# Optimization experiments

Hardware: AMD Instinct MI355X
Metric: run time of the kernel (lower is better)

Reference implementation:

```python
import jax, jax.numpy as jnp
import numpy as np
from jax import lax

VALUE_RANGE = (0.0, 1.0)
NUM_PARAMS = 1
ENC_DIM = 256


def conv2d(x, W, b, stride, pad):
    y = lax.conv_general_dilated(x, W, (stride, stride), [(pad, pad), (pad, pad)],
                                 dimension_numbers=("NCHW", "OIHW", "NCHW"))
    return y + b[None, :, None, None]


def min_pool2d(x, r):
    # torch: -max_pool2d(-x, k=2r+1, stride=1, pad=r)  == min pool padded with +inf
    k = 2 * r + 1
    return lax.reduce_window(x, jnp.inf, lax.min, (1, 1, k, k), (1, 1, 1, 1),
                             padding=[(0, 0), (0, 0), (r, r), (r, r)])


def setup_inputs() -> dict:
    key = jax.random.key(0)
    ks = jax.random.split(key, 10)
    x = jax.random.uniform(ks[0], (16, 3, 512, 512), dtype=jnp.float32)
    latent_out = jax.random.normal(ks[1], (16, ENC_DIM, 32, 32), dtype=jnp.float32)
    W1 = jax.random.normal(ks[2], (ENC_DIM // 2, ENC_DIM, 3, 3), dtype=jnp.float32) * 0.02
    b1 = jnp.zeros((ENC_DIM // 2,), jnp.float32)
    W2 = jax.random.normal(ks[3], (NUM_PARAMS, ENC_DIM // 2, 3, 3), dtype=jnp.float32) * 0.05
    b2 = jnp.zeros((NUM_PARAMS,), jnp.float32)
    W3 = jax.random.normal(ks[4], (NUM_PARAMS, NUM_PARAMS, 1, 1), dtype=jnp.float32) * 0.5
    b3 = jnp.zeros((NUM_PARAMS,), jnp.float32)
    return {"x": x, "latent_out": latent_out, "W1": W1, "b1": b1,
            "W2": W2, "b2": b2, "W3": W3, "b3": b3}


def reference(x, latent_out, W1, b1, W2, b2, W3, b3):
    n, c, H, W = x.shape
    # ---- params_predictor ----
    h = conv2d(latent_out, W1, b1, 2, 1)
    h = jnp.where(h >= 0, h, 0.02 * h)  # LeakyReLU(0.02)
    h = conv2d(h, W2, b2, 2, 1)
    h = h.mean(axis=(2, 3), keepdims=True)  # AdaptiveAvgPool2d(1)
    h = conv2d(h, W3, b3, 1, 0)
    params = jnp.tanh(h)  # [n, 1, 1, 1]
    lo, hi = VALUE_RANGE
    params = params * (hi - lo) / 2 + (hi + lo) / 2

    # ---- dark channel (r=0) + atmospheric light A via top-k gather-mean ----
    dark = x.min(axis=1)  # [n, H, W]
    length = H * W
    num = max(int(length * 0.001), 1)
    dc_vec = dark.reshape(n, -1)
    _, idx = lax.top_k(dc_vec, num)  # brightest dark-channel pixels
    imvec = x.transpose(0, 2, 3, 1).reshape(n, length, c)  # [n, HW, 3]
    A = jnp.take_along_axis(imvec, idx[:, :, None], axis=1).mean(axis=1)  # [n, 3]

    # ---- transmission map ----
    A4 = A[:, :, None, None]
    dc2 = (x / A4).min(axis=1, keepdims=True)  # [n, 1, H, W]
    dc2 = min_pool2d(dc2, r=3)
    T = 1.0 - params * dc2
    T = jnp.repeat(T, 3, axis=1)
    T = jnp.maximum(T, 0.01)

    out = (x - A4) / T + A4
    out = (out - out.min()) / (out.max() - out.min())
    return out


if __name__ == "__main__":
    inp = setup_inputs()
    o = jax.jit(reference)(**inp)
    print(o.shape, o.dtype)
```

## Files before the change

### kernel.cpp

```cpp
#include <hip/hip_runtime.h>
#include <math.h>

#define FINF 3.0e38f

typedef __attribute__((ext_vector_type(8))) short short8v;
typedef __attribute__((ext_vector_type(4))) float float4v;

__device__ __forceinline__ unsigned short f2bf(float f) {
  unsigned u = __float_as_uint(f);
  unsigned r = u + 0x7FFFu + ((u >> 16) & 1u);
  return (unsigned short)(r >> 16);
}

__global__ void k_prep(const float* __restrict__ w1, unsigned short* __restrict__ wt2,
                       unsigned* __restrict__ hist, int* __restrict__ cnt) {
  const int idx = blockIdx.x * 256 + threadIdx.x;
  if (idx < 294912) {
    const int ic = idx & 255;
    const int r = idx >> 8;
    const int oc = r & 127;
    const int tap = r >> 7;
    wt2[idx] = f2bf(w1[((size_t)oc * 256 + ic) * 9 + tap]);
  }
  if (idx < 16 * 4096) hist[idx] = 0u;
  if (idx < 16) cnt[idx] = 0;
}

__global__ __launch_bounds__(512) void k_conv1m(const float* __restrict__ lat,
                                                const unsigned short* __restrict__ wt2,
                                                float* __restrict__ h1part) {
  const int b = blockIdx.x, ks = blockIdx.y, nh = blockIdx.z;
  const int t = threadIdx.x;
  __shared__ unsigned short sA[1025 * 40];
  {
    const float4* src = (const float4*)lat + ((size_t)b * 256 + ks * 32) * 256;
#pragma unroll
    for (int i = t; i < 8192; i += 512) {
      const int ic = i >> 8;
      const int q = i & 255;
      const float4 v = src[ic * 256 + q];
      const int px0 = q * 4;
      sA[(px0 + 0) * 40 + ic] = f2bf(v.x);
      sA[(px0 + 1) * 40 + ic] = f2bf(v.y);
      sA[(px0 + 2) * 40 + ic] = f2bf(v.z);
      sA[(px0 + 3) * 40 + ic] = f2bf(v.w);
    }
    if (t < 40) sA[1024 * 40 + t] = 0;
  }
  __syncthreads();

  const int lane = t & 63, wid = t >> 6;
  const int ocbase = nh * 64 + (wid & 1) * 32;
  const int pxbase = (wid >> 1) * 64;
  const int l15 = lane & 15, lg = lane >> 4;

  float4v acc[2][4];
#pragma unroll
  for (int f = 0; f < 2; ++f)
#pragma unroll
    for (int g = 0; g < 4; ++g) acc[f][g] = (float4v){0.f, 0.f, 0.f, 0.f};

#pragma unroll
  for (int tap = 0; tap < 9; ++tap) {
    const int ky = tap / 3, kx = tap % 3;
    short8v aW[2];
#pragma unroll
    for (int f = 0; f < 2; ++f) {
      const int oc = ocbase + f * 16 + l15;
      aW[f] = *(const short8v*)(wt2 + (size_t)(tap * 128 + oc) * 256 + ks * 32 + lg * 8);
    }
    short8v bL[4];
#pragma unroll
    for (int g = 0; g < 4; ++g) {
      const int px = pxbase + g * 16 + l15;
      const int iy = 2 * (px >> 4) - 1 + ky;
      const int ix = 2 * (px & 15) - 1 + kx;
      const int p = (iy >= 0 && ix >= 0) ? iy * 32 + ix : 1024;
      bL[g] = *(const short8v*)(sA + p * 40 + lg * 8);
    }
#pragma unroll
    for (int f = 0; f < 2; ++f)
#pragma unroll
      for (int g = 0; g < 4; ++g)
        acc[f][g] = __builtin_amdgcn_mfma_f32_16x16x32_bf16(aW[f], bL[g], acc[f][g], 0, 0, 0);
  }

  float* dst = h1part + (size_t)ks * 524288 + (size_t)b * 32768;
#pragma unroll
  for (int f = 0; f < 2; ++f)
#pragma unroll
    for (int g = 0; g < 4; ++g)
#pragma unroll
      for (int r = 0; r < 4; ++r) {
        const int oc = ocbase + f * 16 + lg * 4 + r;
        const int px = pxbase + g * 16 + l15;
        dst[oc * 256 + px] = acc[f][g][r];
      }
}

__global__ void k_combine(const float* __restrict__ h1p, float* __restrict__ h1,
                          const float* __restrict__ b1) {
  const int i = blockIdx.x * 256 + threadIdx.x;
  const float4* p = (const float4*)h1p;
  float4 a = p[i];
#pragma unroll
  for (int ks = 1; ks < 8; ++ks) {
    const float4 q = p[(size_t)ks * 131072 + i];
    a.x += q.x; a.y += q.y; a.z += q.z; a.w += q.w;
  }
  const int oc = (i >> 6) & 127;
  const float bias = b1[oc];
  float s;
  s = a.x + bias; a.x = s >= 0.f ? s : 0.02f * s;
  s = a.y + bias; a.y = s >= 0.f ? s : 0.02f * s;
  s = a.z + bias; a.z = s >= 0.f ? s : 0.02f * s;
  s = a.w + bias; a.w = s >= 0.f ? s : 0.02f * s;
  ((float4*)h1)[i] = a;
}

__global__ __launch_bounds__(256) void k_hist(const float* __restrict__ x,
                                              unsigned* __restrict__ ghist,
                                              float* __restrict__ dc) {
  const int lid = blockIdx.x;
  const int b = (lid & 7) | (((lid >> 3) & 1) << 3);
  const int blk = lid >> 4;
  const int t = threadIdx.x;
  __shared__ unsigned lh[4096];
  for (int i = t; i < 4096; i += 256) lh[i] = 0u;
  __syncthreads();
  const float* xr = x + (size_t)b * 3 * 262144;
  const float* xg = xr + 262144;
  const float* xb = xg + 262144;
  float4* dcb = (float4*)(dc + (size_t)b * 262144);
  const int f0 = blk * 2048;
#pragma unroll
  for (int i = 0; i < 8; ++i) {
    const int f4 = f0 + t + i * 256;
    const float4 r = ((const float4*)xr)[f4];
    const float4 g = ((const float4*)xg)[f4];
    const float4 bl = ((const float4*)xb)[f4];
    float4 d4;
    d4.x = fminf(fminf(r.x, g.x), bl.x); atomicAdd(&lh[min(4095, (int)(d4.x * 4096.f))], 1u);
    d4.y = fminf(fminf(r.y, g.y), bl.y); atomicAdd(&lh[min(4095, (int)(d4.y * 4096.f))], 1u);
    d4.z = fminf(fminf(r.z, g.z), bl.z); atomicAdd(&lh[min(4095, (int)(d4.z * 4096.f))], 1u);
    d4.w = fminf(fminf(r.w, g.w), bl.w); atomicAdd(&lh[min(4095, (int)(d4.w * 4096.f))], 1u);
    dcb[f4] = d4;
  }
  __syncthreads();
  for (int i = t; i < 4096; i += 256)
    if (lh[i]) atomicAdd(&ghist[b * 4096 + i], lh[i]);
}

__global__ __launch_bounds__(256) void k_c2col(const float* __restrict__ h1,
                                               const float* __restrict__ w2,
                                               float* __restrict__ psum,
                                               const float* __restrict__ x,
                                               const float* __restrict__ dc,
                                               const unsigned* __restrict__ ghist,
                                               int* __restrict__ cnt,
                                               float* __restrict__ candv,
                                               int* __restrict__ candi,
                                               float* __restrict__ bsums) {
  __shared__ union {
    struct { float sW[72]; float red[256]; } a;
    struct { unsigned h[4096]; unsigned csum[256]; float red[256]; int sB; } c;
  } sm;
  const int t = threadIdx.x;

  if (blockIdx.x < 256) {
    const int b = blockIdx.x & 15, icg = blockIdx.x >> 4;
    const int icbase = icg * 8;
    for (int i = t; i < 72; i += 256) sm.a.sW[i] = w2[icbase * 9 + i];
    __syncthreads();
    const int px = t & 63, sub = t >> 6;
    const int oy = px >> 3, ox = px & 7;
    float s = 0.f;
#pragma unroll
    for (int ii = 0; ii < 2; ++ii) {
      const int icl = sub * 2 + ii;
      const float* hp = h1 + ((size_t)b * 128 + icbase + icl) * 256;
      const float* wp = sm.a.sW + icl * 9;
#pragma unroll
      for (int ky = 0; ky < 3; ++ky) {
        const int iy = 2 * oy - 1 + ky;
        if (iy < 0) continue;
#pragma unroll
        for (int kx = 0; kx < 3; ++kx) {
          const int ix = 2 * ox - 1 + kx;
          if (ix < 0) continue;
          s += wp[ky * 3 + kx] * hp[iy * 16 + ix];
        }
      }
    }
    sm.a.red[t] = s;
    __syncthreads();
    for (int off = 128; off > 0; off >>= 1) {
      if (t < off) sm.a.red[t] += sm.a.red[t + off];
      __syncthreads();
    }
    if (t == 0) psum[b * 16 + icg] = sm.a.red[0];
    return;
  }

  const int lid = blockIdx.x - 256;
  const int b = (lid & 7) | (((lid >> 3) & 1) << 3);
  const int blk = lid >> 4;
  for (int i = t; i < 4096; i += 256) sm.c.h[i] = ghist[b * 4096 + i];
  __syncthreads();
  const int top = 4095 - 16 * t;
  unsigned s = 0;
#pragma unroll
  for (int k = 0; k < 16; ++k) s += sm.c.h[top - k];
  sm.c.csum[t] = s;
  __syncthreads();
  for (int off = 1; off < 256; off <<= 1) {
    const unsigned add = (t >= off) ? sm.c.csum[t - off] : 0u;
    __syncthreads();
    sm.c.csum[t] += add;
    __syncthreads();
  }
  {
    const unsigned incl = sm.c.csum[t];
    const unsigned before = incl - s;
    if (before < 262u && incl >= 262u) {
      unsigned cum = before;
      for (int k = 0; k < 16; ++k) {
        const unsigned c = sm.c.h[top - k];
        if (cum + c >= 262u) { sm.c.sB = top - k; break; }
        cum += c;
      }
    }
  }
  __syncthreads();
  const int B = sm.c.sB;
  const float* xr = x + (size_t)b * 3 * 262144;
  const float* xg = xr + 262144;
  const float* xb = xg + 262144;
  const float4* dcb = (const float4*)(dc + (size_t)b * 262144);
  const int f0 = blk * 2048;
  float s0 = 0.f, s1 = 0.f, s2 = 0.f;
#pragma unroll
  for (int i = 0; i < 8; ++i) {
    const int f4 = f0 + t + i * 256;
    const float4 d4 = dcb[f4];
    const float dv[4] = {d4.x, d4.y, d4.z, d4.w};
#pragma unroll
    for (int j = 0; j < 4; ++j) {
      const int bin = min(4095, (int)(dv[j] * 4096.f));
      if (bin >= B) {
        const int idx = f4 * 4 + j;
        if (bin > B) {
          s0 += xr[idx]; s1 += xg[idx]; s2 += xb[idx];
        } else {
          const int k = atomicAdd(&cnt[b], 1);
          if (k < 4096) { candv[b * 4096 + k] = dv[j]; candi[b * 4096 + k] = idx; }
        }
      }
    }
  }
  sm.c.red[t] = s0; __syncthreads();
  for (int off = 128; off > 0; off >>= 1) { if (t < off) sm.c.red[t] += sm.c.red[t + off]; __syncthreads(); }
  if (t == 0) bsums[((size_t)b * 32 + blk) * 3 + 0] = sm.c.red[0];
  __syncthreads();
  sm.c.red[t] = s1; __syncthreads();
  for (int off = 128; off > 0; off >>= 1) { if (t < off) sm.c.red[t] += sm.c.red[t + off]; __syncthreads(); }
  if (t == 0) bsums[((size_t)b * 32 + blk) * 3 + 1] = sm.c.red[0];
  __syncthreads();
  sm.c.red[t] = s2; __syncthreads();
  for (int off = 128; off > 0; off >>= 1) { if (t < off) sm.c.red[t] += sm.c.red[t + off]; __syncthreads(); }
  if (t == 0) bsums[((size_t)b * 32 + blk) * 3 + 2] = sm.c.red[0];
}

__global__ void k_finalA(const float* __restrict__ x, const float* __restrict__ bsums,
                         const int* __restrict__ cnt, const unsigned* __restrict__ ghist,
                         const float* __restrict__ candv, const int* __restrict__ candi,
                         const float* __restrict__ psum, const float* __restrict__ b2,
                         const float* __restrict__ w3, const float* __restrict__ b3,
                         float* __restrict__ params, float* __restrict__ Av) {
  const int b = blockIdx.x;
  const int t = threadIdx.x;
  __shared__ float sv[4096];
  __shared__ int si[4096];
  __shared__ int sR;
  {
    float p = (t < 16) ? psum[b * 16 + t] : 0.f;
#pragma unroll
    for (int off = 8; off > 0; off >>= 1) p += __shfl_xor(p, off);
    if (t == 0) {
      const float mean = p / 64.f + b2[0];
      const float h = w3[0] * mean + b3[0];
      params[b] = tanhf(h) * 0.5f + 0.5f;
    }
  }
  {
    const int base = 4095 - 64 * t;
    unsigned ssum = 0;
    for (int k = 0; k < 64; ++k) ssum += ghist[b * 4096 + base - k];
    unsigned incl = ssum;
    for (int off = 1; off < 64; off <<= 1) {
      const unsigned v = __shfl_up(incl, off);
      if (t >= off) incl += v;
    }
    const unsigned before = incl - ssum;
    if (before < 262u && incl >= 262u) {
      unsigned cum = before;
      for (int k = 0; k < 64; ++k) {
        const unsigned c = ghist[b * 4096 + base - k];
        if (cum + c >= 262u) { sR = (int)(262u - cum); break; }
        cum += c;
      }
    }
  }
  float S0 = 0.f, S1 = 0.f, S2 = 0.f;
  if (t < 32) {
    S0 = bsums[((size_t)b * 32 + t) * 3 + 0];
    S1 = bsums[((size_t)b * 32 + t) * 3 + 1];
    S2 = bsums[((size_t)b * 32 + t) * 3 + 2];
  }
#pragma unroll
  for (int off = 32; off > 0; off >>= 1) {
    S0 += __shfl_xor(S0, off);
    S1 += __shfl_xor(S1, off);
    S2 += __shfl_xor(S2, off);
  }
  const int n = min(cnt[b], 4096);
  for (int i = t; i < n; i += 64) { sv[i] = candv[b * 4096 + i]; si[i] = candi[b * 4096 + i]; }
  __syncthreads();
  const int r = sR;
  const float* xr = x + (size_t)b * 3 * 262144;
  const float* xg = xr + 262144;
  const float* xb = xg + 262144;
  for (int sel = 0; sel < r; ++sel) {
    float bv = -1.f; int bi = 0x7FFFFFFF; int bx = -1;
    for (int i = t; i < n; i += 64) {
      const float v = sv[i];
      const int id = si[i];
      if (v > bv || (v == bv && id < bi)) { bv = v; bi = id; bx = i; }
    }
#pragma unroll
    for (int off = 32; off > 0; off >>= 1) {
      const float ov = __shfl_xor(bv, off);
      const int oid = __shfl_xor(bi, off);
      const int obx = __shfl_xor(bx, off);
      if (ov > bv || (ov == bv && oid < bi)) { bv = ov; bi = oid; bx = obx; }
    }
    if (bx < 0) break;
    if (t == 0) {
      sv[bx] = -1.f;
      S0 += xr[bi]; S1 += xg[bi]; S2 += xb[bi];
    }
    __syncthreads();
  }
  if (t == 0) {
    Av[b * 3 + 0] = S0 / 262.f;
    Av[b * 3 + 1] = S1 / 262.f;
    Av[b * 3 + 2] = S2 / 262.f;
  }
}

__global__ __launch_bounds__(256) void k_dchv(const float* __restrict__ x,
                                              const float* __restrict__ Av,
                                              const float* __restrict__ params,
                                              float* __restrict__ vm,
                                              float2* __restrict__ pmm) {
  const int lid = blockIdx.x;
  const int swz = (lid & 7) * 128 + (lid >> 3);
  const int b = swz >> 6;
  const int y0 = (swz & 63) * 8;
  const int t = threadIdx.x;
  __shared__ float dcrow2[2][520];
  __shared__ float hmin[14][512];
  const float a0 = Av[b * 3 + 0], a1 = Av[b * 3 + 1], a2 = Av[b * 3 + 2];
  const float pb = params[b];
  const float* xb = x + (size_t)b * 3 * 262144;
  float* vmb = vm + (size_t)b * 262144;
  float lmin = FINF, lmax = -FINF;
  const int half = t >> 7;
  const int c0 = (t & 127) * 4;
#pragma unroll 1
  for (int d = 0; d < 7; ++d) {
    const int i = 2 * d + half;
    const int row = y0 - 3 + i;
    const bool valid = (row >= 0) && (row < 512);
    if (valid) {
      const float4 r  = *(const float4*)(xb + (size_t)row * 512 + c0);
      const float4 g  = *(const float4*)(xb + 262144 + (size_t)row * 512 + c0);
      const float4 bl = *(const float4*)(xb + 524288 + (size_t)row * 512 + c0);
      float* dr = dcrow2[half];
      dr[3 + c0 + 0] = fminf(fminf(r.x / a0, g.x / a1), bl.x / a2);
      dr[3 + c0 + 1] = fminf(fminf(r.y / a0, g.y / a1), bl.y / a2);
      dr[3 + c0 + 2] = fminf(fminf(r.z / a0, g.z / a1), bl.z / a2);
      dr[3 + c0 + 3] = fminf(fminf(r.w / a0, g.w / a1), bl.w / a2);
      if (c0 == 0) {
        dr[0] = FINF; dr[1] = FINF; dr[2] = FINF;
        dr[515] = FINF; dr[516] = FINF; dr[517] = FINF;
      }
    }
    __syncthreads();
    {
      float* hm = hmin[i];
      if (valid) {
        const float* dr = dcrow2[half];
#pragma unroll
        for (int k2 = 0; k2 < 4; ++k2) {
          float m = dr[c0 + k2];
#pragma unroll
          for (int k = 1; k < 7; ++k) m = fminf(m, dr[c0 + k2 + k]);
          hm[c0 + k2] = m;
        }
      } else {
#pragma unroll
        for (int k2 = 0; k2 < 4; ++k2) hm[c0 + k2] = FINF;
      }
    }
    __syncthreads();
    if (d >= 3) {
#pragma unroll
      for (int jj = 0; jj < 2; ++jj) {
        const int j = 2 * (d - 3) + jj;
        const int y = y0 + j;
        float2 v = ((const float2*)hmin[j])[t];
#pragma unroll
        for (int k = 1; k < 7; ++k) {
          const float2 h2 = ((const float2*)hmin[j + k])[t];
          v.x = fminf(v.x, h2.x);
          v.y = fminf(v.y, h2.y);
        }
        ((float2*)(vmb + (size_t)y * 512))[t] = v;
        const float T0 = fmaxf(1.f - pb * v.x, 0.01f);
        const float T1 = fmaxf(1.f - pb * v.y, 0.01f);
        const float i0 = 1.f / T0;
        const float i1 = 1.f / T1;
#pragma unroll
        for (int c = 0; c < 3; ++c) {
          const float a = (c == 0) ? a0 : ((c == 1) ? a1 : a2);
          const float2 xv = ((const float2*)(xb + (size_t)c * 262144 + (size_t)y * 512))[t];
          const float o0 = fmaf(xv.x - a, i0, a);
          const float o1 = fmaf(xv.y - a, i1, a);
          lmin = fminf(lmin, fminf(o0, o1));
          lmax = fmaxf(lmax, fmaxf(o0, o1));
        }
      }
    }
  }
  __shared__ float red[256];
  red[t] = lmin; __syncthreads();
  for (int off = 128; off > 0; off >>= 1) { if (t < off) red[t] = fminf(red[t], red[t + off]); __syncthreads(); }
  const float bmin = red[0];
  __syncthreads();
  red[t] = lmax; __syncthreads();
  for (int off = 128; off > 0; off >>= 1) { if (t < off) red[t] = fmaxf(red[t], red[t + off]); __syncthreads(); }
  if (t == 0) pmm[lid] = make_float2(bmin, red[0]);
}

__global__ __launch_bounds__(256) void k_norm2(const float* __restrict__ x,
                                               const float* __restrict__ vm,
                                               const float* __restrict__ params,
                                               const float* __restrict__ Av,
                                               const float2* __restrict__ pmm,
                                               float* __restrict__ out) {
  const int t = threadIdx.x;
  __shared__ float rmn[256], rmx[256];
  float mn, sc;
  {
    float m0 = FINF, m1 = -FINF;
    for (int i = t; i < 1024; i += 256) {
      const float2 v = pmm[i];
      m0 = fminf(m0, v.x);
      m1 = fmaxf(m1, v.y);
    }
    rmn[t] = m0; rmx[t] = m1;
    __syncthreads();
    for (int off = 128; off > 0; off >>= 1) {
      if (t < off) {
        rmn[t] = fminf(rmn[t], rmn[t + off]);
        rmx[t] = fmaxf(rmx[t], rmx[t + off]);
      }
      __syncthreads();
    }
    mn = rmn[0];
    sc = 1.f / (rmx[0] - mn);
  }
  const int lid = blockIdx.x;
  const int swz = (lid & 7) * 512 + (lid >> 3);
  const int b = swz >> 8;
  const int y = (swz & 255) * 2 + (t >> 7);
  const int c0 = (t & 127) * 4;
  const float pb = params[b];
  const float a0 = Av[b * 3 + 0], a1 = Av[b * 3 + 1], a2 = Av[b * 3 + 2];
  const float4 v = *(const float4*)(vm + (size_t)b * 262144 + (size_t)y * 512 + c0);
  const float i0 = 1.f / fmaxf(1.f - pb * v.x, 0.01f);
  const float i1 = 1.f / fmaxf(1.f - pb * v.y, 0.01f);
  const float i2 = 1.f / fmaxf(1.f - pb * v.z, 0.01f);
  const float i3 = 1.f / fmaxf(1.f - pb * v.w, 0.01f);
  const size_t rowoff = (size_t)b * 3 * 262144 + (size_t)y * 512 + c0;
#pragma unroll
  for (int c = 0; c < 3; ++c) {
    const float a = (c == 0) ? a0 : ((c == 1) ? a1 : a2);
    const float4 xv = *(const float4*)(x + rowoff + (size_t)c * 262144);
    float4 o;
    o.x = (fmaf(xv.x - a, i0, a) - mn) * sc;
    o.y = (fmaf(xv.y - a, i1, a) - mn) * sc;
    o.z = (fmaf(xv.z - a, i2, a) - mn) * sc;
    o.w = (fmaf(xv.w - a, i3, a) - mn) * sc;
    *(float4*)(out + rowoff + (size_t)c * 262144) = o;
  }
}

extern "C" void kernel_launch(void* const* d_in, const int* in_sizes, int n_in,
                              void* d_out, int out_size, void* d_ws, size_t ws_size,
                              hipStream_t stream) {
  const float* x   = (const float*)d_in[0];
  const float* lat = (const float*)d_in[1];
  const float* w1  = (const float*)d_in[2];
  const float* b1  = (const float*)d_in[3];
  const float* w2  = (const float*)d_in[4];
  const float* b2  = (const float*)d_in[5];
  const float* w3  = (const float*)d_in[6];
  const float* b3  = (const float*)d_in[7];
  float* out = (float*)d_out;

  char* ws = (char*)d_ws;
  size_t off = 0;
  auto alloc = [&](size_t sz) -> void* {
    off = (off + 255) & ~(size_t)255;
    void* p = ws + off;
    off += sz;
    return p;
  };
  float*    big   = (float*)alloc((size_t)16 * 512 * 512 * sizeof(float));
  float*    h1p   = big;
  float*    dc    = big;
  float*    vmm   = big;
  float*    h1    = (float*)alloc(524288 * sizeof(float));
  unsigned short* wt2 = (unsigned short*)alloc(294912 * sizeof(unsigned short));
  float*    paramsp = (float*)alloc(16 * sizeof(float));
  float*    psum  = (float*)alloc(16 * 16 * sizeof(float));
  unsigned* hist  = (unsigned*)alloc(16 * 4096 * sizeof(unsigned));
  int*      cnt   = (int*)alloc(16 * sizeof(int));
  float*    bsums = (float*)alloc(16 * 32 * 3 * sizeof(float));
  float*    candv = (float*)alloc(16 * 4096 * sizeof(float));
  int*      candi = (int*)alloc(16 * 4096 * sizeof(int));
  float*    Av    = (float*)alloc(16 * 3 * sizeof(float));
  float2*   pmm   = (float2*)alloc(1024 * sizeof(float2));

  k_prep<<<1152, 256, 0, stream>>>(w1, wt2, hist, cnt);
  k_conv1m<<<dim3(16, 8, 2), 512, 0, stream>>>(lat, wt2, h1p);
  k_combine<<<512, 256, 0, stream>>>(h1p, h1, b1);
  k_hist<<<512, 256, 0, stream>>>(x, hist, dc);
  k_c2col<<<768, 256, 0, stream>>>(h1, w2, psum,
                                   x, dc, hist, cnt, candv, candi, bsums);
  k_finalA<<<16, 64, 0, stream>>>(x, bsums, cnt, hist, candv, candi,
                                  psum, b2, w3, b3, paramsp, Av);
  k_dchv<<<1024, 256, 0, stream>>>(x, Av, paramsp, vmm, pmm);
  k_norm2<<<4096, 256, 0, stream>>>(x, vmm, paramsp, Av, pmm, out);
}
```

Measured before the change: 114.6 us.

## Write unnormalized output in dchv and normalize in place

The dark-channel kernel now computes the full dehazed output directly, with one LDS staging pass and a register-held vertical min. It writes that output instead of storing the min-pooled map for later recomputation. The final kernel becomes a pure in-place affine normalization over the output buffer. This removes the vm buffer and the recomputation from x, but the output is now written twice and read once, which changes total memory traffic.

Result: slower. 118.1 us (+3.1%).

```diff
diff --git a/kernel.cpp b/kernel.cpp
--- a/kernel.cpp
+++ b/kernel.cpp
@@ -361,86 +361,66 @@
 __global__ __launch_bounds__(256) void k_dchv(const float* __restrict__ x,
                                               const float* __restrict__ Av,
                                               const float* __restrict__ params,
-                                              float* __restrict__ vm,
+                                              float* __restrict__ out,
                                               float2* __restrict__ pmm) {
   const int lid = blockIdx.x;
   const int swz = (lid & 7) * 128 + (lid >> 3);
   const int b = swz >> 6;
   const int y0 = (swz & 63) * 8;
   const int t = threadIdx.x;
-  __shared__ float dcrow2[2][520];
-  __shared__ float hmin[14][512];
+  __shared__ float ds[14][520];
   const float a0 = Av[b * 3 + 0], a1 = Av[b * 3 + 1], a2 = Av[b * 3 + 2];
   const float pb = params[b];
   const float* xb = x + (size_t)b * 3 * 262144;
-  float* vmb = vm + (size_t)b * 262144;
+  float* ob = out + (size_t)b * 3 * 262144;
+#pragma unroll 2
+  for (int i = 0; i < 14; ++i) {
+    const int row = y0 - 3 + i;
+    if (row >= 0 && row < 512) {
+      const float2 r  = ((const float2*)(xb + (size_t)row * 512))[t];
+      const float2 g  = ((const float2*)(xb + 262144 + (size_t)row * 512))[t];
+      const float2 bl = ((const float2*)(xb + 524288 + (size_t)row * 512))[t];
+      ds[i][3 + 2 * t]     = fminf(fminf(r.x / a0, g.x / a1), bl.x / a2);
+      ds[i][3 + 2 * t + 1] = fminf(fminf(r.y / a0, g.y / a1), bl.y / a2);
+    } else {
+      ds[i][3 + 2 * t]     = FINF;
+      ds[i][3 + 2 * t + 1] = FINF;
+    }
+    if (t < 3) { ds[i][t] = FINF; ds[i][515 + t] = FINF; }
+  }
+  __syncthreads();
+  float hm0[14], hm1[14];
+#pragma unroll
+  for (int i = 0; i < 14; ++i) {
+    float m0 = ds[i][2 * t], m1 = ds[i][2 * t + 1];
+#pragma unroll
+    for (int k = 1; k < 7; ++k) {
+      m0 = fminf(m0, ds[i][2 * t + k]);
+      m1 = fminf(m1, ds[i][2 * t + 1 + k]);
+    }
+    hm0[i] = m0; hm1[i] = m1;
+  }
   float lmin = FINF, lmax = -FINF;
-  const int half = t >> 7;
-  const int c0 = (t & 127) * 4;
-#pragma unroll 1
-  for (int d = 0; d < 7; ++d) {
-    const int i = 2 * d + half;
-    const int row = y0 - 3 + i;
-    const bool valid = (row >= 0) && (row < 512);
-    if (valid) {
-      const float4 r  = *(const float4*)(xb + (size_t)row * 512 + c0);
-      const float4 g  = *(const float4*)(xb + 262144 + (size_t)row * 512 + c0);
-      const float4 bl = *(const float4*)(xb + 524288 + (size_t)row * 512 + c0);
-      float* dr = dcrow2[half];
-      dr[3 + c0 + 0] = fminf(fminf(r.x / a0, g.x / a1), bl.x / a2);
-      dr[3 + c0 + 1] = fminf(fminf(r.y / a0, g.y / a1), bl.y / a2);
-      dr[3 + c0 + 2] = fminf(fminf(r.z / a0, g.z / a1), bl.z / a2);
-      dr[3 + c0 + 3] = fminf(fminf(r.w / a0, g.w / a1), bl.w / a2);
-      if (c0 == 0) {
-        dr[0] = FINF; dr[1] = FINF; dr[2] = FINF;
-        dr[515] = FINF; dr[516] = FINF; dr[517] = FINF;
-      }
-    }
-    __syncthreads();
-    {
-      float* hm = hmin[i];
-      if (valid) {
-        const float* dr = dcrow2[half];
-#pragma unroll
-        for (int k2 = 0; k2 < 4; ++k2) {
-          float m = dr[c0 + k2];
-#pragma unroll
-          for (int k = 1; k < 7; ++k) m = fminf(m, dr[c0 + k2 + k]);
-          hm[c0 + k2] = m;
-        }
-      } else {
-#pragma unroll
-        for (int k2 = 0; k2 < 4; ++k2) hm[c0 + k2] = FINF;
-      }
-    }
-    __syncthreads();
-    if (d >= 3) {
-#pragma unroll
-      for (int jj = 0; jj < 2; ++jj) {
-        const int j = 2 * (d - 3) + jj;
-        const int y = y0 + j;
-        float2 v = ((const float2*)hmin[j])[t];
-#pragma unroll
-        for (int k = 1; k < 7; ++k) {
-          const float2 h2 = ((const float2*)hmin[j + k])[t];
-          v.x = fminf(v.x, h2.x);
-          v.y = fminf(v.y, h2.y);
-        }
-        ((float2*)(vmb + (size_t)y * 512))[t] = v;
-        const float T0 = fmaxf(1.f - pb * v.x, 0.01f);
-        const float T1 = fmaxf(1.f - pb * v.y, 0.01f);
-        const float i0 = 1.f / T0;
-        const float i1 = 1.f / T1;
-#pragma unroll
-        for (int c = 0; c < 3; ++c) {
-          const float a = (c == 0) ? a0 : ((c == 1) ? a1 : a2);
-          const float2 xv = ((const float2*)(xb + (size_t)c * 262144 + (size_t)y * 512))[t];
-          const float o0 = fmaf(xv.x - a, i0, a);
-          const float o1 = fmaf(xv.y - a, i1, a);
-          lmin = fminf(lmin, fminf(o0, o1));
-          lmax = fmaxf(lmax, fmaxf(o0, o1));
-        }
-      }
+#pragma unroll
+  for (int j = 0; j < 8; ++j) {
+    const int y = y0 + j;
+    float v0 = hm0[j], v1 = hm1[j];
+#pragma unroll
+    for (int k = 1; k < 7; ++k) {
+      v0 = fminf(v0, hm0[j + k]);
+      v1 = fminf(v1, hm1[j + k]);
+    }
+    const float i0 = 1.f / fmaxf(1.f - pb * v0, 0.01f);
+    const float i1 = 1.f / fmaxf(1.f - pb * v1, 0.01f);
+#pragma unroll
+    for (int c = 0; c < 3; ++c) {
+      const float a = (c == 0) ? a0 : ((c == 1) ? a1 : a2);
+      const float2 xv = ((const float2*)(xb + (size_t)c * 262144 + (size_t)y * 512))[t];
+      const float o0 = fmaf(xv.x - a, i0, a);
+      const float o1 = fmaf(xv.y - a, i1, a);
+      lmin = fminf(lmin, fminf(o0, o1));
+      lmax = fmaxf(lmax, fmaxf(o0, o1));
+      ((float2*)(ob + (size_t)c * 262144 + (size_t)y * 512))[t] = make_float2(o0, o1);
     }
   }
   __shared__ float red[256];
@@ -453,12 +433,8 @@
   if (t == 0) pmm[lid] = make_float2(bmin, red[0]);
 }
 
-__global__ __launch_bounds__(256) void k_norm2(const float* __restrict__ x,
-                                               const float* __restrict__ vm,
-                                               const float* __restrict__ params,
-                                               const float* __restrict__ Av,
-                                               const float2* __restrict__ pmm,
-                                               float* __restrict__ out) {
+__global__ __launch_bounds__(256) void k_norm2(float* __restrict__ out,
+                                               const float2* __restrict__ pmm) {
   const int t = threadIdx.x;
   __shared__ float rmn[256], rmx[256];
   float mn, sc;
@@ -481,29 +457,16 @@
     mn = rmn[0];
     sc = 1.f / (rmx[0] - mn);
   }
-  const int lid = blockIdx.x;
-  const int swz = (lid & 7) * 512 + (lid >> 3);
-  const int b = swz >> 8;
-  const int y = (swz & 255) * 2 + (t >> 7);
-  const int c0 = (t & 127) * 4;
-  const float pb = params[b];
-  const float a0 = Av[b * 3 + 0], a1 = Av[b * 3 + 1], a2 = Av[b * 3 + 2];
-  const float4 v = *(const float4*)(vm + (size_t)b * 262144 + (size_t)y * 512 + c0);
-  const float i0 = 1.f / fmaxf(1.f - pb * v.x, 0.01f);
-  const float i1 = 1.f / fmaxf(1.f - pb * v.y, 0.01f);
-  const float i2 = 1.f / fmaxf(1.f - pb * v.z, 0.01f);
-  const float i3 = 1.f / fmaxf(1.f - pb * v.w, 0.01f);
-  const size_t rowoff = (size_t)b * 3 * 262144 + (size_t)y * 512 + c0;
-#pragma unroll
-  for (int c = 0; c < 3; ++c) {
-    const float a = (c == 0) ? a0 : ((c == 1) ? a1 : a2);
-    const float4 xv = *(const float4*)(x + rowoff + (size_t)c * 262144);
-    float4 o;
-    o.x = (fmaf(xv.x - a, i0, a) - mn) * sc;
-    o.y = (fmaf(xv.y - a, i1, a) - mn) * sc;
-    o.z = (fmaf(xv.z - a, i2, a) - mn) * sc;
-    o.w = (fmaf(xv.w - a, i3, a) - mn) * sc;
-    *(float4*)(out + rowoff + (size_t)c * 262144) = o;
+  float4* o4 = (float4*)out;
+  const int base = blockIdx.x * 768 + t;
+#pragma unroll
+  for (int i = 0; i < 3; ++i) {
+    float4 v = o4[base + i * 256];
+    v.x = (v.x - mn) * sc;
+    v.y = (v.y - mn) * sc;
+    v.z = (v.z - mn) * sc;
+    v.w = (v.w - mn) * sc;
+    o4[base + i * 256] = v;
   }
 }
 
@@ -531,7 +494,6 @@
   float*    big   = (float*)alloc((size_t)16 * 512 * 512 * sizeof(float));
   float*    h1p   = big;
   float*    dc    = big;
-  float*    vmm   = big;
   float*    h1    = (float*)alloc(524288 * sizeof(float));
   unsigned short* wt2 = (unsigned short*)alloc(294912 * sizeof(unsigned short));
   float*    paramsp = (float*)alloc(16 * sizeof(float));
@@ -552,6 +514,6 @@
                                    x, dc, hist, cnt, candv, candi, bsums);
   k_finalA<<<16, 64, 0, stream>>>(x, bsums, cnt, hist, candv, candi,
                                   psum, b2, w3, b3, paramsp, Av);
-  k_dchv<<<1024, 256, 0, stream>>>(x, Av, paramsp, vmm, pmm);
-  k_norm2<<<4096, 256, 0, stream>>>(x, vmm, paramsp, Av, pmm, out);
-}
+  k_dchv<<<1024, 256, 0, stream>>>(x, Av, paramsp, out, pmm);
+  k_norm2<<<4096, 256, 0, stream>>>(out, pmm);
+}
```
